# Kernel tuning notes

Hardware: AMD Instinct MI355X
Metric: run time of the kernel (lower is better)

Reference implementation:

```python
import jax, jax.numpy as jnp
import numpy as np

B, L, D, H = 4, 1024, 1024, 16
HD = D // H  # head_dim = 64
SCALE = HD ** -0.5


def setup_inputs() -> dict:
    key = jax.random.key(0)
    k1, k2, k3, k4 = jax.random.split(key, 4)
    x = jax.random.normal(k1, (B, L, D), dtype=jnp.float32)
    # torch nn.Linear(dim, 3*dim): y = x @ W.T + b; we store W already transposed to [D, 3D]
    Wqkv = jax.random.normal(k2, (D, 3 * D), dtype=jnp.float32) * (D ** -0.5)
    bqkv = jax.random.normal(k3, (3 * D,), dtype=jnp.float32) * 0.02
    # distance_embedding: nn.Embedding(2*length - 1, head_dim)
    dist_emb = jax.random.normal(k4, (2 * L - 1, HD), dtype=jnp.float32) * 0.02
    return {"x": x, "Wqkv": Wqkv, "bqkv": bqkv, "dist_emb": dist_emb}


def reference(x, Wqkv, bqkv, dist_emb):
    b, l, d = x.shape
    # QKV projection -> [3, B, H, L, HD]
    qkv = (x @ Wqkv + bqkv).reshape(b, l, 3, H, HD).transpose(2, 0, 3, 1, 4)
    q, k, v = qkv[0], qkv[1], qkv[2]
    # raw attention scores: [B, H, L, L]
    scores = jnp.einsum("bhld,bhmd->bhlm", q, k)
    # relative position bias (relative_key_query branch)
    pos = jnp.arange(l)
    distance = pos[:, None] - pos[None, :]          # [L, L] in [-(L-1), L-1]
    pe = dist_emb[distance + (L - 1)]               # [L, L, HD]
    rel_q = jnp.einsum("bhld,lrd->bhlr", q, pe)
    rel_k = jnp.einsum("bhrd,lrd->bhlr", k, pe)
    scores = (scores + rel_q + rel_k) * SCALE
    probs = jax.nn.softmax(scores, axis=-1)
    out = jnp.einsum("bhlm,bhmd->bhld", probs, v)   # [B, H, L, HD]
    return out.transpose(0, 2, 1, 3).reshape(b, l, d)
```

## Files before the change

kernel.cpp:

```cpp
#include <hip/hip_runtime.h>
#include <hip/hip_bf16.h>
#include <math.h>

#define Bq 4
#define Lq 1024
#define Dq 1024
#define Hq 16
#define HDq 64
#define BHq (Bq * Hq)
#define HEAD_ELEMS ((size_t)BHq * Lq * HDq)

typedef short bf16x8 __attribute__((ext_vector_type(8)));
typedef _Float16 f16x8 __attribute__((ext_vector_type(8)));
typedef float f32x4 __attribute__((ext_vector_type(4)));
#define MFMA16B(A, B, C) __builtin_amdgcn_mfma_f32_16x16x32_bf16(A, B, C, 0, 0, 0)
#define MFMA16F(A, B, C) __builtin_amdgcn_mfma_f32_16x16x32_f16(A, B, C, 0, 0, 0)

#if __has_builtin(__builtin_amdgcn_exp2f)
#define EXP2F(x) __builtin_amdgcn_exp2f(x)
#else
#define EXP2F(x) __expf((x) * 0.6931471805599453f)
#endif

__device__ __forceinline__ unsigned short f2bf(float x) {
  unsigned u = __builtin_bit_cast(unsigned, x);
  unsigned r = u + 0x7FFFu + ((u >> 16) & 1u);
  return (unsigned short)(r >> 16);
}
__device__ __forceinline__ float bf2f(unsigned short s) {
  unsigned u = ((unsigned)s) << 16;
  return __builtin_bit_cast(float, u);
}
__device__ __forceinline__ unsigned short f2h(float x) {
  _Float16 h = (_Float16)x;
  return __builtin_bit_cast(unsigned short, h);
}

__global__ __launch_bounds__(256) void prep_all(
    const float* __restrict__ X, unsigned short* __restrict__ Xh,
    const float* __restrict__ W, unsigned short* __restrict__ Wt,
    const float* __restrict__ e, unsigned short* __restrict__ o) {
  __shared__ unsigned short tile[64 * 72];
  const int bid = blockIdx.x;
  const int tid = threadIdx.x;
  if (bid < 4096) {
    size_t i = (size_t)bid * 256 + tid;
    float4 f = *(const float4*)(X + i * 4);
    uint2 pk;
    pk.x = (unsigned)f2h(f.x) | ((unsigned)f2h(f.y) << 16);
    pk.y = (unsigned)f2h(f.z) | ((unsigned)f2h(f.w) << 16);
    *(uint2*)(Xh + i * 4) = pk;
  } else if (bid < 4864) {
    const int wb = bid - 4096;
    const int k0 = (wb & 15) * 64;
    const int n0 = (wb >> 4) * 64;
#pragma unroll
    for (int it = 0; it < 4; it++) {
      int idx = tid + it * 256;
      int r = idx >> 4, c4 = (idx & 15) * 4;
      float4 f = *(const float4*)(W + (size_t)(k0 + r) * 3072 + n0 + c4);
      unsigned w0 = (unsigned)f2h(f.x) | ((unsigned)f2h(f.y) << 16);
      unsigned w1 = (unsigned)f2h(f.z) | ((unsigned)f2h(f.w) << 16);
      *(unsigned*)&tile[r * 72 + c4] = w0;
      *(unsigned*)&tile[r * 72 + c4 + 2] = w1;
    }
    __syncthreads();
#pragma unroll
    for (int it = 0; it < 4; it++) {
      int u = tid + it * 256;
      int n = u >> 4, k4 = (u & 15) * 4;
      unsigned short e0 = tile[(k4 + 0) * 72 + n];
      unsigned short e1 = tile[(k4 + 1) * 72 + n];
      unsigned short e2 = tile[(k4 + 2) * 72 + n];
      unsigned short e3 = tile[(k4 + 3) * 72 + n];
      uint2 pk;
      pk.x = (unsigned)e0 | ((unsigned)e1 << 16);
      pk.y = (unsigned)e2 | ((unsigned)e3 << 16);
      *(uint2*)(Wt + (size_t)(n0 + n) * 1024 + k0 + k4) = pk;
    }
  } else {
    int i = (bid - 4864) * 256 + tid;
    if (i < 2047 * 64) {
      int row = i >> 6, c = i & 63;
      o[(row << 6) | (c ^ ((row & 7) << 3))] = f2bf(e[i]);
    }
  }
}

__global__ __launch_bounds__(256, 2) void qkv_mfma(
    const unsigned short* __restrict__ Xh, const unsigned short* __restrict__ Wt,
    const float* __restrict__ bias, unsigned short* __restrict__ qkvg,
    unsigned short* __restrict__ vtg) {
  __shared__ __align__(16) char smem[32768];
  unsigned short* Asm = (unsigned short*)smem;
  unsigned short* Bsm = (unsigned short*)(smem + 8192);
  unsigned short* Cs  = (unsigned short*)smem;

  const int tid = threadIdx.x;
  const int w = tid >> 6, lane = tid & 63;
  const int col = lane & 15, quad = lane >> 4;
  const int wm = (w >> 1) * 64, wn = (w & 1) * 64;
  const int bn = blockIdx.x * 128, bm = blockIdx.y * 128;

  const unsigned short* Ag = Xh + (size_t)bm * 1024;
  const unsigned short* Bg = Wt + (size_t)bn * 1024;
  const int ldrow = w * 32 + (lane >> 2);
  const int ldoff = (lane & 3) * 8;

  f32x4 acc[4][4];
#pragma unroll
  for (int i = 0; i < 4; i++)
#pragma unroll
    for (int j = 0; j < 4; j++) acc[i][j] = (f32x4){0.f, 0.f, 0.f, 0.f};

  for (int k0 = 0; k0 < 1024; k0 += 32) {
    __syncthreads();
#pragma unroll
    for (int it = 0; it < 2; it++) {
      const unsigned short* ga = Ag + (size_t)(ldrow + it * 16) * 1024 + k0 + ldoff;
      const unsigned short* gb = Bg + (size_t)(ldrow + it * 16) * 1024 + k0 + ldoff;
      __builtin_amdgcn_global_load_lds(
          (const __attribute__((address_space(1))) unsigned*)ga,
          (__attribute__((address_space(3))) unsigned*)(Asm + (w * 32 + it * 16) * 32),
          16, 0, 0);
      __builtin_amdgcn_global_load_lds(
          (const __attribute__((address_space(1))) unsigned*)gb,
          (__attribute__((address_space(3))) unsigned*)(Bsm + (w * 32 + it * 16) * 32),
          16, 0, 0);
    }
    __syncthreads();
    f16x8 af[4], bf[4];
#pragma unroll
    for (int i = 0; i < 4; i++)
      af[i] = *(const f16x8*)&Asm[(wm + i * 16 + col) * 32 + quad * 8];
#pragma unroll
    for (int j = 0; j < 4; j++)
      bf[j] = *(const f16x8*)&Bsm[(wn + j * 16 + col) * 32 + quad * 8];
#pragma unroll
    for (int i = 0; i < 4; i++)
#pragma unroll
      for (int j = 0; j < 4; j++)
        acc[i][j] = MFMA16F(af[i], bf[j], acc[i][j]);
  }

  float bj[4];
#pragma unroll
  for (int j = 0; j < 4; j++) bj[j] = bias[bn + wn + j * 16 + col];

  __syncthreads();
#pragma unroll
  for (int i = 0; i < 4; i++)
#pragma unroll
    for (int j = 0; j < 4; j++)
#pragma unroll
      for (int k = 0; k < 4; k++) {
        int row = wm + i * 16 + quad * 4 + k;
        int c = wn + j * 16 + col;
        Cs[row * 128 + (c ^ ((row & 7) << 3))] = f2bf(acc[i][j][k] + bj[j]);
      }
  __syncthreads();

  const int t = bn >> 10;
  if (t != 2) {
    unsigned short* dst_base = qkvg + (size_t)t * HEAD_ELEMS;
#pragma unroll
    for (int it = 0; it < 8; it++) {
      int u = tid + it * 256;
      int row = u >> 4, c8 = (u & 15) * 8;
      int m = bm + row;
      int n = bn + c8;
      int b = m >> 10, l = m & 1023;
      int cc = n & 1023, h = cc >> 6;
      int d0 = (cc & 63) ^ ((l & 7) << 3);
      uint4 val = *(const uint4*)&Cs[row * 128 + (c8 ^ ((row & 7) << 3))];
      *(uint4*)(dst_base + (((size_t)(b * 16 + h) * 1024 + l) * 64 + d0)) = val;
    }
  } else {
    const int b = bm >> 10, lblk = bm & 1023;
    const int h0 = (bn & 1023) >> 6;
#pragma unroll
    for (int it = 0; it < 16; it++) {
      int u = tid + it * 256;
      int hh = u >> 11;
      int rem = u & 2047;
      int cc2 = rem >> 10;
      int rem2 = rem & 1023;
      int d = rem2 >> 4;
      int r4 = (rem2 & 15) * 4;
      int c = hh * 64 + d;
      int rb = cc2 * 64 + r4;
      unsigned short e0 = Cs[(rb + 0) * 128 + (c ^ (((rb + 0) & 7) << 3))];
      unsigned short e1 = Cs[(rb + 1) * 128 + (c ^ (((rb + 1) & 7) << 3))];
      unsigned short e2 = Cs[(rb + 2) * 128 + (c ^ (((rb + 2) & 7) << 3))];
      unsigned short e3 = Cs[(rb + 3) * 128 + (c ^ (((rb + 3) & 7) << 3))];
      uint2 pk;
      pk.x = (unsigned)e0 | ((unsigned)e1 << 16);
      pk.y = (unsigned)e2 | ((unsigned)e3 << 16);
      int r4s = r4 ^ ((d & 7) << 3);
      size_t bh = (size_t)(b * 16 + h0 + hh);
      *(uint2*)(vtg + bh * ((size_t)HDq * Lq) + (size_t)d * Lq + lblk + cc2 * 64 + r4s) = pk;
    }
  }
}

__global__ __launch_bounds__(256, 2) void attn_mfma(
    const unsigned short* __restrict__ qg, const unsigned short* __restrict__ kg,
    const unsigned short* __restrict__ vtg, const unsigned short* __restrict__ emb,
    float* __restrict__ out) {
  __shared__ __align__(16) char smem[41984];
  unsigned short* Ks  = (unsigned short*)smem;
  unsigned short* VTs = (unsigned short*)(smem + 8192);
  unsigned short* Pb  = (unsigned short*)(smem + 16384);
  unsigned short* Ps  = Pb;
  unsigned short* B12 = (unsigned short*)(smem + 24576);

  const int bh = blockIdx.x;
  const int l0 = blockIdx.y * 64;
  const int tid = threadIdx.x;
  const int w = tid >> 6, lane = tid & 63;
  const int col = lane & 15, quad = lane >> 4;
  const int lw = w * 16;
  const int fo = quad * 8;
  const int swm = (col & 7) << 3;

  const unsigned short* Qg = qg + ((size_t)bh * Lq + l0) * HDq;
  const unsigned short* Kp = kg + (size_t)bh * Lq * HDq;
  const unsigned short* Vp = vtg + (size_t)bh * HDq * Lq;

  bf16x8 qf[2];
#pragma unroll
  for (int ks = 0; ks < 2; ks++)
    qf[ks] = *(const bf16x8*)(Qg + (size_t)(lw + col) * 64 + ((fo + ks * 32) ^ swm));

  bf16x8 sav[4][2];
#pragma unroll
  for (int dm = 0; dm < 4; dm++) {
    int g = l0 + 1024 + dm * 16 + col;
    g = (g > 2046) ? 2046 : g;
    int m = (g & 7) << 3;
#pragma unroll
    for (int ks = 0; ks < 2; ks++)
      sav[dm][ks] = *(const bf16x8*)(emb + (size_t)g * 64 + ((fo + ks * 32) ^ m));
  }

  f32x4 oacc[4];
#pragma unroll
  for (int nt = 0; nt < 4; nt++) oacc[nt] = (f32x4){0.f, 0.f, 0.f, 0.f};
  float mrow[4] = {-1e30f, -1e30f, -1e30f, -1e30f};
  float lrow[4] = {0.f, 0.f, 0.f, 0.f};

  int pb0 = l0 + 960;
  const int lr8 = (lane & 7) * 8;

  for (int ch = 0; ch < 16; ch++) {
    __syncthreads();

#pragma unroll
    for (int it = 0; it < 2; it++) {
      const int rb = w * 16 + it * 8;
      const int r = rb + (lane >> 3);
      __builtin_amdgcn_global_load_lds(
          (const __attribute__((address_space(1))) unsigned*)(Kp + (size_t)r * 64 + lr8),
          (__attribute__((address_space(3))) unsigned*)(Ks + rb * 64), 16, 0, 0);
      __builtin_amdgcn_global_load_lds(
          (const __attribute__((address_space(1))) unsigned*)(Vp + (size_t)r * Lq + lr8),
          (__attribute__((address_space(3))) unsigned*)(VTs + rb * 64), 16, 0, 0);
      __builtin_amdgcn_global_load_lds(
          (const __attribute__((address_space(1))) unsigned*)(emb + (size_t)(pb0 + r) * 64 + lr8),
          (__attribute__((address_space(3))) unsigned*)(Pb + rb * 64), 16, 0, 0);
    }
    __syncthreads();

    bf16x8 kf[4][2];
#pragma unroll
    for (int rt = 0; rt < 4; rt++)
#pragma unroll
      for (int ks = 0; ks < 2; ks++)
        kf[rt][ks] = *(const bf16x8*)&Ks[((rt * 16 + col) << 6) + ((fo + ks * 32) ^ swm)];
    f32x4 sac[4];
#pragma unroll
    for (int rt = 0; rt < 4; rt++) {
      f32x4 z = (f32x4){0.f, 0.f, 0.f, 0.f};
      z = MFMA16B(qf[0], kf[rt][0], z);
      z = MFMA16B(qf[1], kf[rt][1], z);
      sac[rt] = z;
    }

    bf16x8 kaf[2];
#pragma unroll
    for (int ks = 0; ks < 2; ks++)
      kaf[ks] = *(const bf16x8*)&Ks[((lw + col) << 6) + ((fo + ks * 32) ^ swm)];

    bf16x8 fresh[4][2];
#pragma unroll
    for (int dm = 0; dm < 4; dm++)
#pragma unroll
      for (int ks = 0; ks < 2; ks++)
        fresh[dm][ks] = *(const bf16x8*)&Pb[((dm * 16 + col) << 6) + ((fo + ks * 32) ^ swm)];

#pragma unroll
    for (int dt = 0; dt < 8; dt++) {
      bf16x8 pbf0 = (dt < 4) ? fresh[dt & 3][0] : sav[dt & 3][0];
      bf16x8 pbf1 = (dt < 4) ? fresh[dt & 3][1] : sav[dt & 3][1];
      f32x4 z = (f32x4){0.f, 0.f, 0.f, 0.f};
      f32x4 y = (f32x4){0.f, 0.f, 0.f, 0.f};
      z = MFMA16B(qf[0], pbf0, z);
      z = MFMA16B(qf[1], pbf1, z);
      y = MFMA16B(kaf[0], pbf0, y);
      y = MFMA16B(kaf[1], pbf1, y);
      const int dcol = dt * 16 + col;
#pragma unroll
      for (int k = 0; k < 4; k++) {
        int l1 = lw + quad * 4 + k;
        int r1 = l1 - dcol + 63;
        if (r1 >= 0 && r1 < 64) B12[l1 * 136 + 2 * r1] = f2bf(z[k]);
        int r2 = lw + quad * 4 + k;
        int l2 = dcol - 63 + r2;
        if (l2 >= 0 && l2 < 64) B12[l2 * 136 + 2 * r2 + 1] = f2bf(y[k]);
      }
    }
#pragma unroll
    for (int dm = 0; dm < 4; dm++)
#pragma unroll
      for (int ks = 0; ks < 2; ks++)
        sav[dm][ks] = fresh[dm][ks];
    __syncthreads();

    float p[4][4];
    float alpha[4];
#pragma unroll
    for (int k = 0; k < 4; k++) {
      int l1 = lw + quad * 4 + k;
      float st[4];
#pragma unroll
      for (int rt = 0; rt < 4; rt++) {
        int r = rt * 16 + col;
        unsigned pr = *(const unsigned*)&B12[l1 * 136 + 2 * r];
        float bias = bf2f((unsigned short)(pr & 0xFFFFu)) +
                     bf2f((unsigned short)(pr >> 16));
        st[rt] = (sac[rt][k] + bias) * 0.18033688011112042f;
      }
      float mx = fmaxf(fmaxf(st[0], st[1]), fmaxf(st[2], st[3]));
      mx = fmaxf(mx, __shfl_xor(mx, 1));
      mx = fmaxf(mx, __shfl_xor(mx, 2));
      mx = fmaxf(mx, __shfl_xor(mx, 4));
      mx = fmaxf(mx, __shfl_xor(mx, 8));
      float mnew = fmaxf(mrow[k], mx);
      float a = EXP2F(mrow[k] - mnew);
      mrow[k] = mnew;
      alpha[k] = a;
      float ls = 0.f;
#pragma unroll
      for (int rt = 0; rt < 4; rt++) {
        p[rt][k] = EXP2F(st[rt] - mnew);
        ls += p[rt][k];
      }
      lrow[k] = lrow[k] * a + ls;
    }
#pragma unroll
    for (int nt = 0; nt < 4; nt++)
#pragma unroll
      for (int k = 0; k < 4; k++) oacc[nt][k] *= alpha[k];

#pragma unroll
    for (int rt = 0; rt < 4; rt++)
#pragma unroll
      for (int k = 0; k < 4; k++) {
        int l1 = lw + quad * 4 + k;
        Ps[(l1 << 6) + ((rt * 16 + col) ^ ((l1 & 7) << 3))] = f2bf(p[rt][k]);
      }

    bf16x8 pf[2];
#pragma unroll
    for (int ks = 0; ks < 2; ks++)
      pf[ks] = *(const bf16x8*)&Ps[((lw + col) << 6) + ((fo + ks * 32) ^ swm)];
#pragma unroll
    for (int nt = 0; nt < 4; nt++) {
      bf16x8 v0 = *(const bf16x8*)&VTs[((nt * 16 + col) << 6) + (fo ^ swm)];
      bf16x8 v1 = *(const bf16x8*)&VTs[((nt * 16 + col) << 6) + ((fo + 32) ^ swm)];
      oacc[nt] = MFMA16B(pf[0], v0, oacc[nt]);
      oacc[nt] = MFMA16B(pf[1], v1, oacc[nt]);
    }

    Kp += 64 * 64;
    Vp += 64;
    pb0 -= 64;
  }

  float inv[4];
#pragma unroll
  for (int k = 0; k < 4; k++) {
    float t = lrow[k];
    t += __shfl_xor(t, 1);
    t += __shfl_xor(t, 2);
    t += __shfl_xor(t, 4);
    t += __shfl_xor(t, 8);
    inv[k] = 1.0f / t;
  }
  const int b = bh >> 4, h = bh & 15;
#pragma unroll
  for (int nt = 0; nt < 4; nt++) {
#pragma unroll
    for (int k = 0; k < 4; k++) {
      int lg = l0 + lw + quad * 4 + k;
      int d = nt * 16 + col;
      out[(((size_t)b * Lq + lg) * Hq + h) * HDq + d] = oacc[nt][k] * inv[k];
    }
  }
}

extern "C" void kernel_launch(void* const* d_in, const int* in_sizes, int n_in,
                              void* d_out, int out_size, void* d_ws, size_t ws_size,
                              hipStream_t stream) {
  const float* x        = (const float*)d_in[0];
  const float* Wqkv     = (const float*)d_in[1];
  const float* bqkv     = (const float*)d_in[2];
  const float* dist_emb = (const float*)d_in[3];
  float* out = (float*)d_out;

  unsigned short* Xh   = (unsigned short*)d_ws;
  unsigned short* Wt   = (unsigned short*)((char*)d_ws + (8u << 20));
  unsigned short* qkvg = (unsigned short*)((char*)d_ws + (16u << 20));
  unsigned short* vtg  = (unsigned short*)((char*)d_ws + (40u << 20));
  unsigned short* emb  = (unsigned short*)((char*)d_ws + (48u << 20));

  prep_all<<<dim3(5376), dim3(256), 0, stream>>>(x, Xh, Wqkv, Wt, dist_emb, emb);

  qkv_mfma<<<dim3(24, 32), dim3(256), 0, stream>>>(Xh, Wt, bqkv, qkvg, vtg);

  attn_mfma<<<dim3(BHq, Lq / 64), dim3(256), 0, stream>>>(
      qkvg, qkvg + HEAD_ELEMS, vtg, emb, out);
}
```

Before: 246.6 us.

## Double-buffer K, V and distance-embedding tiles in LDS for load/compute overlap

The attention kernel now keeps two LDS buffers for the K, V^T and relative-position embedding tiles. While the current chunk is being computed, the async global-to-LDS loads for the next chunk are issued, which removes one barrier per iteration and hides load latency behind MFMA work. Ps and B12 move to their own regions, so the probability scratch no longer aliases the embedding buffer. LDS per block grows to about 73 KB, which still fits two blocks per CU but leaves little headroom.

New measurement: 248.6 us. No clear change (+0.8%).

```diff
diff --git a/kernel.cpp b/kernel.cpp
--- a/kernel.cpp
+++ b/kernel.cpp
@@ -207,12 +207,9 @@
     const unsigned short* __restrict__ qg, const unsigned short* __restrict__ kg,
     const unsigned short* __restrict__ vtg, const unsigned short* __restrict__ emb,
     float* __restrict__ out) {
-  __shared__ __align__(16) char smem[41984];
-  unsigned short* Ks  = (unsigned short*)smem;
-  unsigned short* VTs = (unsigned short*)(smem + 8192);
-  unsigned short* Pb  = (unsigned short*)(smem + 16384);
-  unsigned short* Ps  = Pb;
-  unsigned short* B12 = (unsigned short*)(smem + 24576);
+  __shared__ __align__(16) char smem[74752];
+  unsigned short* Ps  = (unsigned short*)(smem + 49152);
+  unsigned short* B12 = (unsigned short*)(smem + 57344);
 
   const int bh = blockIdx.x;
   const int l0 = blockIdx.y * 64;
@@ -227,6 +224,29 @@
   const unsigned short* Kp = kg + (size_t)bh * Lq * HDq;
   const unsigned short* Vp = vtg + (size_t)bh * HDq * Lq;
 
+  const int lr8 = (lane & 7) * 8;
+
+  auto STAGE = [&](int buf, const unsigned short* Kpp, const unsigned short* Vpp,
+                   int pbb) {
+    unsigned short* Kd = (unsigned short*)(smem + buf * 24576);
+    unsigned short* Vd = (unsigned short*)(smem + buf * 24576 + 8192);
+    unsigned short* Pd = (unsigned short*)(smem + buf * 24576 + 16384);
+#pragma unroll
+    for (int it = 0; it < 2; it++) {
+      const int rb = w * 16 + it * 8;
+      const int r = rb + (lane >> 3);
+      __builtin_amdgcn_global_load_lds(
+          (const __attribute__((address_space(1))) unsigned*)(Kpp + (size_t)r * 64 + lr8),
+          (__attribute__((address_space(3))) unsigned*)(Kd + rb * 64), 16, 0, 0);
+      __builtin_amdgcn_global_load_lds(
+          (const __attribute__((address_space(1))) unsigned*)(Vpp + (size_t)r * Lq + lr8),
+          (__attribute__((address_space(3))) unsigned*)(Vd + rb * 64), 16, 0, 0);
+      __builtin_amdgcn_global_load_lds(
+          (const __attribute__((address_space(1))) unsigned*)(emb + (size_t)(pbb + r) * 64 + lr8),
+          (__attribute__((address_space(3))) unsigned*)(Pd + rb * 64), 16, 0, 0);
+    }
+  };
+
   bf16x8 qf[2];
 #pragma unroll
   for (int ks = 0; ks < 2; ks++)
@@ -250,33 +270,25 @@
   float lrow[4] = {0.f, 0.f, 0.f, 0.f};
 
   int pb0 = l0 + 960;
-  const int lr8 = (lane & 7) * 8;
+
+  STAGE(0, Kp, Vp, pb0);
 
   for (int ch = 0; ch < 16; ch++) {
+    const int cur = ch & 1;
+    unsigned short* Ksc = (unsigned short*)(smem + cur * 24576);
+    unsigned short* VTc = (unsigned short*)(smem + cur * 24576 + 8192);
+    unsigned short* Pbc = (unsigned short*)(smem + cur * 24576 + 16384);
+
     __syncthreads();
 
-#pragma unroll
-    for (int it = 0; it < 2; it++) {
-      const int rb = w * 16 + it * 8;
-      const int r = rb + (lane >> 3);
-      __builtin_amdgcn_global_load_lds(
-          (const __attribute__((address_space(1))) unsigned*)(Kp + (size_t)r * 64 + lr8),
-          (__attribute__((address_space(3))) unsigned*)(Ks + rb * 64), 16, 0, 0);
-      __builtin_amdgcn_global_load_lds(
-          (const __attribute__((address_space(1))) unsigned*)(Vp + (size_t)r * Lq + lr8),
-          (__attribute__((address_space(3))) unsigned*)(VTs + rb * 64), 16, 0, 0);
-      __builtin_amdgcn_global_load_lds(
-          (const __attribute__((address_space(1))) unsigned*)(emb + (size_t)(pb0 + r) * 64 + lr8),
-          (__attribute__((address_space(3))) unsigned*)(Pb + rb * 64), 16, 0, 0);
-    }
-    __syncthreads();
+    if (ch < 15) STAGE(cur ^ 1, Kp + 4096, Vp + 64, pb0 - 64);
 
     bf16x8 kf[4][2];
 #pragma unroll
     for (int rt = 0; rt < 4; rt++)
 #pragma unroll
       for (int ks = 0; ks < 2; ks++)
-        kf[rt][ks] = *(const bf16x8*)&Ks[((rt * 16 + col) << 6) + ((fo + ks * 32) ^ swm)];
+        kf[rt][ks] = *(const bf16x8*)&Ksc[((rt * 16 + col) << 6) + ((fo + ks * 32) ^ swm)];
     f32x4 sac[4];
 #pragma unroll
     for (int rt = 0; rt < 4; rt++) {
@@ -289,14 +301,14 @@
     bf16x8 kaf[2];
 #pragma unroll
     for (int ks = 0; ks < 2; ks++)
-      kaf[ks] = *(const bf16x8*)&Ks[((lw + col) << 6) + ((fo + ks * 32) ^ swm)];
+      kaf[ks] = *(const bf16x8*)&Ksc[((lw + col) << 6) + ((fo + ks * 32) ^ swm)];
 
     bf16x8 fresh[4][2];
 #pragma unroll
     for (int dm = 0; dm < 4; dm++)
 #pragma unroll
       for (int ks = 0; ks < 2; ks++)
-        fresh[dm][ks] = *(const bf16x8*)&Pb[((dm * 16 + col) << 6) + ((fo + ks * 32) ^ swm)];
+        fresh[dm][ks] = *(const bf16x8*)&Pbc[((dm * 16 + col) << 6) + ((fo + ks * 32) ^ swm)];
 
 #pragma unroll
     for (int dt = 0; dt < 8; dt++) {
@@ -376,8 +388,8 @@
       pf[ks] = *(const bf16x8*)&Ps[((lw + col) << 6) + ((fo + ks * 32) ^ swm)];
 #pragma unroll
     for (int nt = 0; nt < 4; nt++) {
-      bf16x8 v0 = *(const bf16x8*)&VTs[((nt * 16 + col) << 6) + (fo ^ swm)];
-      bf16x8 v1 = *(const bf16x8*)&VTs[((nt * 16 + col) << 6) + ((fo + 32) ^ swm)];
+      bf16x8 v0 = *(const bf16x8*)&VTc[((nt * 16 + col) << 6) + (fo ^ swm)];
+      bf16x8 v1 = *(const bf16x8*)&VTc[((nt * 16 + col) << 6) + ((fo + 32) ^ swm)];
       oacc[nt] = MFMA16B(pf[0], v0, oacc[nt]);
       oacc[nt] = MFMA16B(pf[1], v1, oacc[nt]);
     }
```
